# Optimization experiments

Hardware: AMD Instinct MI355X
Metric: run time of the kernel (lower is better)

## Reference

```python
import jax, jax.numpy as jnp
import numpy as np

E = 400000   # total edges
G = 64       # num graphs
H = 256      # hidden_dim
NN = 20000   # node id range
FRONTIER_BONUS = 0.5


def layer_norm(x, g, b, eps=1e-5):
    m = jnp.mean(x, axis=-1, keepdims=True)
    v = jnp.var(x, axis=-1, keepdims=True)
    return (x - m) / jnp.sqrt(v + eps) * g + b


def setup_inputs() -> dict:
    key = jax.random.key(0)
    ks = jax.random.split(key, 20)
    s = 0.02
    inp = {
        "edge_tokens": jax.random.normal(ks[0], (E, H), jnp.float32),
        "question_tokens": jax.random.normal(ks[1], (G, H), jnp.float32),
        "edge_batch": jnp.sort(jax.random.randint(ks[2], (E,), 0, G)),
        "selected_mask": jax.random.bernoulli(ks[3], 0.3, (E,)),
        "edge_heads": jax.random.randint(ks[4], (E,), 0, NN),
        "edge_tails": jax.random.randint(ks[5], (E,), 0, NN),
        "current_tail": jax.random.randint(ks[6], (G,), 0, NN),
        # edge_proj params: LayerNorm(H+2) -> Linear(H+2,H) -> GELU -> Linear(H,H) -> GELU
        "ln1_g": jnp.ones((H + 2,), jnp.float32),
        "ln1_b": jnp.zeros((H + 2,), jnp.float32),
        "W1": s * jax.random.normal(ks[7], (H + 2, H), jnp.float32),
        "b1": jnp.zeros((H,), jnp.float32),
        "W2": s * jax.random.normal(ks[8], (H, H), jnp.float32),
        "b2": jnp.zeros((H,), jnp.float32),
        # selection_head: Linear(H,1)
        "sel_w": s * jax.random.normal(ks[9], (H, 1), jnp.float32),
        "sel_b": jnp.zeros((1,), jnp.float32),
        # stop_head: LayerNorm(2H) -> Linear(2H,H) -> GELU -> Linear(H,1)
        "ln2_g": jnp.ones((2 * H,), jnp.float32),
        "ln2_b": jnp.zeros((2 * H,), jnp.float32),
        "sW1": s * jax.random.normal(ks[10], (2 * H, H), jnp.float32),
        "sb1": jnp.zeros((H,), jnp.float32),
        "sW2": s * jax.random.normal(ks[11], (H, 1), jnp.float32),
        "sb2": jnp.zeros((1,), jnp.float32),
    }
    return inp


def reference(edge_tokens, question_tokens, edge_batch, selected_mask,
              edge_heads, edge_tails, current_tail,
              ln1_g, ln1_b, W1, b1, W2, b2, sel_w, sel_b,
              ln2_g, ln2_b, sW1, sb1, sW2, sb2):
    num_graphs = question_tokens.shape[0]
    candidate = ~selected_mask
    cur_e = current_tail[edge_batch]                       # [E] gather by graph id
    frontier = candidate & ((edge_heads == cur_e) | (edge_tails == cur_e))
    aux = jnp.stack([candidate.astype(jnp.float32), frontier.astype(jnp.float32)], axis=-1)
    x = jnp.concatenate([edge_tokens, aux], axis=-1)       # [E, H+2]
    h = layer_norm(x, ln1_g, ln1_b)
    h = jax.nn.gelu(h @ W1 + b1, approximate=False)        # Dropout is identity in eval
    h = jax.nn.gelu(h @ W2 + b2, approximate=False)        # edge_repr [E, H]
    edge_logits = (h @ sel_w)[:, 0] + sel_b[0]
    edge_logits = edge_logits + FRONTIER_BONUS * frontier.astype(jnp.float32)
    counts = jax.ops.segment_sum(jnp.ones((h.shape[0],), jnp.float32), edge_batch, num_segments=num_graphs)
    counts = jnp.clip(counts, 1.0)                          # bincount.clamp(min=1)
    pooled = jax.ops.segment_sum(h, edge_batch, num_segments=num_graphs) / counts[:, None]
    s_in = jnp.concatenate([pooled, question_tokens], axis=-1)  # [G, 2H]
    s = layer_norm(s_in, ln2_g, ln2_b)
    s = jax.nn.gelu(s @ sW1 + sb1, approximate=False)
    stop_logits = (s @ sW2)[:, 0] + sb2[0]
    return edge_logits, stop_logits, pooled
```

## Files before the change

### kernel.cpp

```cpp
#include <hip/hip_runtime.h>
#include <hip/hip_bf16.h>
#include <cstdint>


typedef __bf16 bf16x8 __attribute__((ext_vector_type(8)));
typedef float  f32x4  __attribute__((ext_vector_type(4)));

__device__ __forceinline__ float gelu_f(float x) {
  float x2 = x * x;
  float t1 = __builtin_fmaf(0.1029444f, x2, 2.3022078f);
  float a  = x * t1;
  float e;
  asm("v_exp_f32 %0, %1" : "=v"(e) : "v"(a));
  float r;
  asm("v_rcp_f32 %0, %1" : "=v"(r) : "v"(e + 1.0f));
  return x - x * r;
}

__device__ __forceinline__ bf16x8 as_frag(uint4 u) {
  union { uint4 u; bf16x8 f; } c; c.u = u; return c.f;
}

__global__ void prep_pack(const float* __restrict__ W1, const float* __restrict__ W2,
                          const float* __restrict__ ln1g,
                          __bf16* __restrict__ W1p, __bf16* __restrict__ W2p) {
  int gid = blockIdx.x * blockDim.x + threadIdx.x;
  int m  = gid >> 13;
  int b  = (gid >> 6) & 127;
  int l  = gid & 63;
  int kt = b >> 4, nt = b & 15;
  int k0 = kt * 32 + ((l >> 4) << 3);
  int n  = nt * 16 + (l & 15);
  const float* W = m ? W2 : W1;
  bf16x8 v;
#pragma unroll
  for (int i = 0; i < 8; ++i) {
    int k = k0 + i;
    float wv = W[k * 256 + n];
    if (!m) wv *= ln1g[k];
    v[i] = (__bf16)wv;
  }
  __bf16* dst = m ? W2p : W1p;
  *(bf16x8*)(dst + (size_t)(b * 64 + l) * 8) = v;
}

__global__ void prep_vec(const float* __restrict__ W1, const float* __restrict__ ln1g,
                         const float* __restrict__ ln1b, const float* __restrict__ b1,
                         const unsigned* __restrict__ smask_words,
                         float* __restrict__ C0, float* __restrict__ GW6,
                         float* __restrict__ GW7, int* __restrict__ maskIsByte) {
  __shared__ float red[4][256];
  const int n = threadIdx.x & 255, c = threadIdx.x >> 8;
  const int k0 = c * 64, k1 = (c == 3) ? 258 : k0 + 64;
  float s = 0.f;
#pragma unroll 4
  for (int k = k0; k < k1; ++k) s += ln1b[k] * W1[k * 256 + n];
  red[c][n] = s;
  __syncthreads();
  if (c == 0) {
    C0[n]  = b1[n] + red[0][n] + red[1][n] + red[2][n] + red[3][n];
    GW6[n] = ln1g[256] * W1[256 * 256 + n];
    GW7[n] = ln1g[257] * W1[257 * 256 + n];
  }
  if (threadIdx.x == 0) {
    int big = 0;
    for (int i = 0; i < 64; ++i) { if (smask_words[i] > 1u) big = 1; }
    *maskIsByte = big;
  }
}

#define EPB 64

__device__ __forceinline__ void gemm8_reg(const char* __restrict__ Wp,
                                          const char* aBase, unsigned swA,
                                          unsigned gA, int bOff,
                                          f32x4 (&acc)[4][4]) {
  uint4 bv[4], bn[4];
#pragma unroll
  for (int cf = 0; cf < 4; ++cf)
    bv[cf] = *(const uint4*)(Wp + bOff + (cf << 10));
#pragma unroll
  for (int kt = 0; kt < 8; ++kt) {
    if (kt < 7) {
#pragma unroll
      for (int cf = 0; cf < 4; ++cf)
        bn[cf] = *(const uint4*)(Wp + (kt + 1) * 16384 + bOff + (cf << 10));
    }
    bf16x8 av[4];
#pragma unroll
    for (int rf = 0; rf < 4; ++rf)
      av[rf] = *(const bf16x8*)(aBase + rf * 8192 + (((unsigned)(kt * 64) + gA) ^ swA));
#pragma unroll
    for (int rf = 0; rf < 4; ++rf)
#pragma unroll
      for (int cf = 0; cf < 4; ++cf)
        acc[rf][cf] = __builtin_amdgcn_mfma_f32_16x16x32_bf16(av[rf], as_frag(bv[cf]),
                                                              acc[rf][cf], 0, 0, 0);
#pragma unroll
    for (int cf = 0; cf < 4; ++cf) bv[cf] = bn[cf];
  }
}

__global__ __launch_bounds__(256, 3) void edge_kernel(
    const float* __restrict__ tok, const int* __restrict__ ebatch,
    const unsigned char* __restrict__ smaskB,
    const int* __restrict__ eheads, const int* __restrict__ etails,
    const int* __restrict__ curtail,
    const __bf16* __restrict__ W1p, const __bf16* __restrict__ W2p,
    const float* __restrict__ C0v, const float* __restrict__ GW6v,
    const float* __restrict__ GW7v, const float* __restrict__ b2v,
    const float* __restrict__ selwv, const float* __restrict__ selbv,
    const int* __restrict__ maskFlag,
    float* __restrict__ outLogits, float* __restrict__ pooledAcc,
    float* __restrict__ cnts) {
  __shared__ __align__(16) char As_[64 * 512];
  __shared__ float sZa0[64], sZa1[64], sFront[64];
  __shared__ float sLog[64][4];
  __shared__ int sG[64];

  const int t = threadIdx.x;
  const int w = t >> 6, l = t & 63;
  const int base = blockIdx.x * EPB;

  if (t < 64) {
    int ge = base + t;
    int g  = ebatch[ge];
    int mb = *maskFlag;
    int mv = mb ? (int)smaskB[ge] : ((const int*)smaskB)[ge];
    int cand = (mv == 0);
    int cur  = curtail[g];
    int fr   = cand && ((eheads[ge] == cur) || (etails[ge] == cur));
    sZa0[t] = (float)cand; sZa1[t] = (float)fr; sFront[t] = (float)fr; sG[t] = g;
  }
  __syncthreads();

  if (t == 0) {
    int cg = sG[0]; float run = 1.f;
    for (int e = 1; e < EPB; ++e) {
      int g = sG[e];
      if (g == cg) run += 1.f;
      else { atomicAdd(&cnts[cg], run); cg = g; run = 1.f; }
    }
    atomicAdd(&cnts[cg], run);
  }

  {
    const int e = t >> 2, q = t & 3;
    const float* rp = tok + (size_t)(base + e) * 256 + q * 4;
    float s = 0.f, s2 = 0.f;
#pragma unroll
    for (int j = 0; j < 16; ++j) {
      float4 v = *(const float4*)(rp + j * 16);
      s  += v.x + v.y + v.z + v.w;
      s2 += v.x * v.x + v.y * v.y + v.z * v.z + v.w * v.w;
    }
    float a0 = 0.f, a1 = 0.f;
    if (q == 0) { a0 = sZa0[e]; a1 = sZa1[e]; s += a0 + a1; s2 += a0 + a1; }
    s  += __shfl_xor(s, 1);  s  += __shfl_xor(s, 2);
    s2 += __shfl_xor(s2, 1); s2 += __shfl_xor(s2, 2);
    const float mean = s * (1.0f / 258.0f);
    const float var  = s2 * (1.0f / 258.0f) - mean * mean;
    const float rstd = rsqrtf(var + 1e-5f);
    const float nm   = -mean * rstd;
    const unsigned sw = (unsigned)(e & 7) << 4;
    const float* rp2 = rp;
    asm volatile("" : "+v"(rp2));
#pragma unroll
    for (int j = 0; j < 16; ++j) {
      float4 v = *(const float4*)(rp2 + j * 16);
      union { __bf16 h[4]; uint2 u; } cv;
      cv.h[0] = (__bf16)__builtin_fmaf(v.x, rstd, nm);
      cv.h[1] = (__bf16)__builtin_fmaf(v.y, rstd, nm);
      cv.h[2] = (__bf16)__builtin_fmaf(v.z, rstd, nm);
      cv.h[3] = (__bf16)__builtin_fmaf(v.w, rstd, nm);
      unsigned off = (unsigned)(q * 8 + j * 32);
      *(uint2*)(As_ + e * 512 + (off ^ sw)) = cv.u;
    }
    if (q == 0) {
      sZa0[e] = __builtin_fmaf(a0, rstd, nm);
      sZa1[e] = __builtin_fmaf(a1, rstd, nm);
    }
  }
  __syncthreads();

  const int rA = l & 15;
  const int r0 = (l >> 4) << 2;
  f32x4 acc[4][4];
  {
    float c0r[4], w6r[4], w7r[4];
#pragma unroll
    for (int cf = 0; cf < 4; ++cf) {
      int col = w * 64 + cf * 16 + rA;
      c0r[cf] = C0v[col]; w6r[cf] = GW6v[col]; w7r[cf] = GW7v[col];
    }
    f32x4 za0q[4], za1q[4];
#pragma unroll
    for (int rf = 0; rf < 4; ++rf) {
      za0q[rf] = *(const f32x4*)&sZa0[rf * 16 + r0];
      za1q[rf] = *(const f32x4*)&sZa1[rf * 16 + r0];
    }
#pragma unroll
    for (int rf = 0; rf < 4; ++rf)
#pragma unroll
      for (int cf = 0; cf < 4; ++cf)
#pragma unroll
        for (int i = 0; i < 4; ++i)
          acc[rf][cf][i] = c0r[cf] + za0q[rf][i] * w6r[cf] + za1q[rf][i] * w7r[cf];
  }

  const unsigned swA = (unsigned)(rA & 7) << 4;
  const unsigned gA  = (unsigned)((l >> 4) << 4);
  const char* aBase  = As_ + rA * 512;
  const int bOff     = (w << 12) + (l << 4);

  gemm8_reg((const char*)W1p, aBase, swA, gA, bOff, acc);
  __syncthreads();

#pragma unroll
  for (int rf = 0; rf < 4; ++rf)
#pragma unroll
    for (int i = 0; i < 4; ++i) {
      int row = rf * 16 + r0 + i;
      char* rowp = As_ + row * 512;
      unsigned sw = (unsigned)(row & 7) << 4;
#pragma unroll
      for (int cf = 0; cf < 4; ++cf) {
        int col = w * 64 + cf * 16 + rA;
        *(__bf16*)(rowp + (((unsigned)(col * 2)) ^ sw)) = (__bf16)gelu_f(acc[rf][cf][i]);
      }
    }
  __syncthreads();

#pragma unroll
  for (int cf = 0; cf < 4; ++cf) {
    float bb = b2v[w * 64 + cf * 16 + rA];
#pragma unroll
    for (int rf = 0; rf < 4; ++rf)
#pragma unroll
      for (int i = 0; i < 4; ++i) acc[rf][cf][i] = bb;
  }
  gemm8_reg((const char*)W2p, aBase, swA, gA, bOff, acc);

#pragma unroll
  for (int rf = 0; rf < 4; ++rf)
#pragma unroll
    for (int cf = 0; cf < 4; ++cf)
#pragma unroll
      for (int i = 0; i < 4; ++i) acc[rf][cf][i] = gelu_f(acc[rf][cf][i]);

  {
    float lwr[4];
#pragma unroll
    for (int cf = 0; cf < 4; ++cf) lwr[cf] = selwv[w * 64 + cf * 16 + rA];
#pragma unroll
    for (int rf = 0; rf < 4; ++rf)
#pragma unroll
      for (int i = 0; i < 4; ++i) {
        float p = acc[rf][0][i] * lwr[0] + acc[rf][1][i] * lwr[1]
                + acc[rf][2][i] * lwr[2] + acc[rf][3][i] * lwr[3];
        p += __shfl_xor(p, 1); p += __shfl_xor(p, 2);
        p += __shfl_xor(p, 4); p += __shfl_xor(p, 8);
        if (rA == 0) sLog[rf * 16 + r0 + i][w] = p;
      }
  }
  __syncthreads();
  if (t < 64)
    outLogits[base + t] = sLog[t][0] + sLog[t][1] + sLog[t][2] + sLog[t][3]
                        + selbv[0] + 0.5f * sFront[t];

  if (sG[0] == sG[EPB - 1]) {
    int g = sG[0];
#pragma unroll
    for (int cf = 0; cf < 4; ++cf) {
      float sv = 0.f;
#pragma unroll
      for (int rf = 0; rf < 4; ++rf)
#pragma unroll
        for (int i = 0; i < 4; ++i) sv += acc[rf][cf][i];
      sv += __shfl_xor(sv, 16);
      sv += __shfl_xor(sv, 32);
      if (l < 16) atomicAdd(&pooledAcc[g * 256 + w * 64 + cf * 16 + l], sv);
    }
  } else {
#pragma unroll
    for (int rf = 0; rf < 4; ++rf)
#pragma unroll
      for (int i = 0; i < 4; ++i) {
        int row = rf * 16 + r0 + i;
        int g = sG[row];
#pragma unroll
        for (int cf = 0; cf < 4; ++cf)
          atomicAdd(&pooledAcc[g * 256 + w * 64 + cf * 16 + rA], acc[rf][cf][i]);
      }
  }
}

__global__ __launch_bounds__(256) void stop_kernel(
    const float* __restrict__ pooledAcc, const float* __restrict__ cnts,
    const float* __restrict__ qtok,
    const float* __restrict__ ln2g, const float* __restrict__ ln2b,
    const float* __restrict__ sW1, const float* __restrict__ sb1,
    const float* __restrict__ sW2, const float* __restrict__ sb2,
    float* __restrict__ outStop, float* __restrict__ outPooled) {
  __shared__ float sIn[512], sLn[512], sRed[8];
  const int t = threadIdx.x, g = blockIdx.x;
  const int w = t >> 6, l = t & 63;
  float c = fmaxf(cnts[g], 1.0f);
  float p = pooledAcc[g * 256 + t] / c;
  outPooled[g * 256 + t] = p;
  sIn[t] = p;
  sIn[256 + t] = qtok[g * 256 + t];
  __syncthreads();
  float a = sIn[t], b = sIn[256 + t];
  float s = a + b, s2 = a * a + b * b;
#pragma unroll
  for (int m = 1; m < 64; m <<= 1) { s += __shfl_xor(s, m); s2 += __shfl_xor(s2, m); }
  if (l == 0) { sRed[w] = s; sRed[4 + w] = s2; }
  __syncthreads();
  s  = sRed[0] + sRed[1] + sRed[2] + sRed[3];
  s2 = sRed[4] + sRed[5] + sRed[6] + sRed[7];
  const float mean = s * (1.0f / 512.0f);
  const float var  = s2 * (1.0f / 512.0f) - mean * mean;
  const float rstd = rsqrtf(var + 1e-5f);
  sLn[t]       = (a - mean) * rstd * ln2g[t] + ln2b[t];
  sLn[256 + t] = (b - mean) * rstd * ln2g[256 + t] + ln2b[256 + t];
  __syncthreads();
  float accv = sb1[t];
#pragma unroll 8
  for (int k = 0; k < 512; ++k) accv += sLn[k] * sW1[k * 256 + t];
  float u = gelu_f(accv);
  float part = u * sW2[t];
#pragma unroll
  for (int m = 1; m < 64; m <<= 1) part += __shfl_xor(part, m);
  if (l == 0) sRed[w] = part;
  __syncthreads();
  if (t == 0) outStop[g] = sRed[0] + sRed[1] + sRed[2] + sRed[3] + sb2[0];
}

extern "C" void kernel_launch(void* const* d_in, const int* in_sizes, int n_in,
                              void* d_out, int out_size, void* d_ws, size_t ws_size,
                              hipStream_t stream) {
  const float* tok   = (const float*)d_in[0];
  const float* qtok  = (const float*)d_in[1];
  const int* ebatch  = (const int*)d_in[2];
  const void* smask  = d_in[3];
  const int* eheads  = (const int*)d_in[4];
  const int* etails  = (const int*)d_in[5];
  const int* curtail = (const int*)d_in[6];
  const float* ln1g  = (const float*)d_in[7];
  const float* ln1b  = (const float*)d_in[8];
  const float* W1    = (const float*)d_in[9];
  const float* b1    = (const float*)d_in[10];
  const float* W2    = (const float*)d_in[11];
  const float* b2    = (const float*)d_in[12];
  const float* selw  = (const float*)d_in[13];
  const float* selb  = (const float*)d_in[14];
  const float* ln2g  = (const float*)d_in[15];
  const float* ln2b  = (const float*)d_in[16];
  const float* sW1   = (const float*)d_in[17];
  const float* sb1   = (const float*)d_in[18];
  const float* sW2   = (const float*)d_in[19];
  const float* sb2   = (const float*)d_in[20];

  const int E = in_sizes[2];
  const int G = in_sizes[1] / 256;

  char* ws = (char*)d_ws;
  __bf16* W1p   = (__bf16*)(ws);
  __bf16* W2p   = (__bf16*)(ws + 131072);
  float*  C0    = (float*)(ws + 262144);
  float*  GW6   = (float*)(ws + 263168);
  float*  GW7   = (float*)(ws + 264192);
  float*  pooled= (float*)(ws + 265216);
  float*  cnts  = (float*)(ws + 330752);
  int*    mflag = (int*)(ws + 331008);
  (void)ws_size; (void)n_in; (void)out_size;

  hipMemsetAsync(ws + 265216, 0, 65536 + 256, stream);

  prep_pack<<<64, 256, 0, stream>>>(W1, W2, ln1g, W1p, W2p);
  prep_vec<<<1, 1024, 0, stream>>>(W1, ln1g, ln1b, b1, (const unsigned*)smask,
                                   C0, GW6, GW7, mflag);
  edge_kernel<<<E / EPB, 256, 0, stream>>>(
      tok, ebatch, (const unsigned char*)smask, eheads, etails, curtail,
      W1p, W2p, C0, GW6, GW7, b2, selw, selb, mflag,
      (float*)d_out, pooled, cnts);
  stop_kernel<<<G, 256, 0, stream>>>(pooled, cnts, qtok, ln2g, ln2b,
                                     sW1, sb1, sW2, sb2,
                                     (float*)d_out + E, (float*)d_out + E + G);
}
```

Measured before the change: 300.5 us.

## Make edge kernel persistent and deepen weight prefetch to two k-steps

The edge kernel becomes a grid-stride persistent kernel with 768 blocks, each looping over 64-edge tiles instead of launching one block per tile. The GEMM inner loop now holds three rotating register buffers, so weight fragments are fetched two k-steps ahead rather than one. The aim is to cut block launch and teardown overhead and hide more global-load latency for the weights. The costs are more VGPRs, which could hurt occupancy at launch bounds of 3 blocks per CU, an extra barrier per tile, and no overlap between tiles within a block.

Result: slower. 764.8 us (+154.5%).

```diff
diff --git a/kernel.cpp b/kernel.cpp
--- a/kernel.cpp
+++ b/kernel.cpp
@@ -75,16 +75,25 @@
                                           const char* aBase, unsigned swA,
                                           unsigned gA, int bOff,
                                           f32x4 (&acc)[4][4]) {
-  uint4 bv[4], bn[4];
-#pragma unroll
-  for (int cf = 0; cf < 4; ++cf)
-    bv[cf] = *(const uint4*)(Wp + bOff + (cf << 10));
+  uint4 b0[4], b1_[4], b2_[4];
+#pragma unroll
+  for (int cf = 0; cf < 4; ++cf) b0[cf]  = *(const uint4*)(Wp + bOff + (cf << 10));
+#pragma unroll
+  for (int cf = 0; cf < 4; ++cf) b1_[cf] = *(const uint4*)(Wp + 16384 + bOff + (cf << 10));
 #pragma unroll
   for (int kt = 0; kt < 8; ++kt) {
-    if (kt < 7) {
-#pragma unroll
-      for (int cf = 0; cf < 4; ++cf)
-        bn[cf] = *(const uint4*)(Wp + (kt + 1) * 16384 + bOff + (cf << 10));
+    if (kt < 6) {
+      const char* pf = Wp + (size_t)(kt + 2) * 16384 + bOff;
+      if ((kt + 2) % 3 == 0) {
+#pragma unroll
+        for (int cf = 0; cf < 4; ++cf) b0[cf]  = *(const uint4*)(pf + (cf << 10));
+      } else if ((kt + 2) % 3 == 1) {
+#pragma unroll
+        for (int cf = 0; cf < 4; ++cf) b1_[cf] = *(const uint4*)(pf + (cf << 10));
+      } else {
+#pragma unroll
+        for (int cf = 0; cf < 4; ++cf) b2_[cf] = *(const uint4*)(pf + (cf << 10));
+      }
     }
     bf16x8 av[4];
 #pragma unroll
@@ -93,11 +102,11 @@
 #pragma unroll
     for (int rf = 0; rf < 4; ++rf)
 #pragma unroll
-      for (int cf = 0; cf < 4; ++cf)
-        acc[rf][cf] = __builtin_amdgcn_mfma_f32_16x16x32_bf16(av[rf], as_frag(bv[cf]),
+      for (int cf = 0; cf < 4; ++cf) {
+        bf16x8 bf = as_frag((kt % 3 == 0) ? b0[cf] : (kt % 3 == 1) ? b1_[cf] : b2_[cf]);
+        acc[rf][cf] = __builtin_amdgcn_mfma_f32_16x16x32_bf16(av[rf], bf,
                                                               acc[rf][cf], 0, 0, 0);
-#pragma unroll
-    for (int cf = 0; cf < 4; ++cf) bv[cf] = bn[cf];
+      }
   }
 }
 
@@ -112,7 +121,7 @@
     const float* __restrict__ selwv, const float* __restrict__ selbv,
     const int* __restrict__ maskFlag,
     float* __restrict__ outLogits, float* __restrict__ pooledAcc,
-    float* __restrict__ cnts) {
+    float* __restrict__ cnts, int nTiles) {
   __shared__ __align__(16) char As_[64 * 512];
   __shared__ float sZa0[64], sZa1[64], sFront[64];
   __shared__ float sLog[64][4];
@@ -120,178 +129,182 @@
 
   const int t = threadIdx.x;
   const int w = t >> 6, l = t & 63;
-  const int base = blockIdx.x * EPB;
-
-  if (t < 64) {
-    int ge = base + t;
-    int g  = ebatch[ge];
-    int mb = *maskFlag;
-    int mv = mb ? (int)smaskB[ge] : ((const int*)smaskB)[ge];
-    int cand = (mv == 0);
-    int cur  = curtail[g];
-    int fr   = cand && ((eheads[ge] == cur) || (etails[ge] == cur));
-    sZa0[t] = (float)cand; sZa1[t] = (float)fr; sFront[t] = (float)fr; sG[t] = g;
-  }
-  __syncthreads();
-
-  if (t == 0) {
-    int cg = sG[0]; float run = 1.f;
-    for (int e = 1; e < EPB; ++e) {
-      int g = sG[e];
-      if (g == cg) run += 1.f;
-      else { atomicAdd(&cnts[cg], run); cg = g; run = 1.f; }
-    }
-    atomicAdd(&cnts[cg], run);
-  }
-
-  {
-    const int e = t >> 2, q = t & 3;
-    const float* rp = tok + (size_t)(base + e) * 256 + q * 4;
-    float s = 0.f, s2 = 0.f;
-#pragma unroll
-    for (int j = 0; j < 16; ++j) {
-      float4 v = *(const float4*)(rp + j * 16);
-      s  += v.x + v.y + v.z + v.w;
-      s2 += v.x * v.x + v.y * v.y + v.z * v.z + v.w * v.w;
-    }
-    float a0 = 0.f, a1 = 0.f;
-    if (q == 0) { a0 = sZa0[e]; a1 = sZa1[e]; s += a0 + a1; s2 += a0 + a1; }
-    s  += __shfl_xor(s, 1);  s  += __shfl_xor(s, 2);
-    s2 += __shfl_xor(s2, 1); s2 += __shfl_xor(s2, 2);
-    const float mean = s * (1.0f / 258.0f);
-    const float var  = s2 * (1.0f / 258.0f) - mean * mean;
-    const float rstd = rsqrtf(var + 1e-5f);
-    const float nm   = -mean * rstd;
-    const unsigned sw = (unsigned)(e & 7) << 4;
-    const float* rp2 = rp;
-    asm volatile("" : "+v"(rp2));
-#pragma unroll
-    for (int j = 0; j < 16; ++j) {
-      float4 v = *(const float4*)(rp2 + j * 16);
-      union { __bf16 h[4]; uint2 u; } cv;
-      cv.h[0] = (__bf16)__builtin_fmaf(v.x, rstd, nm);
-      cv.h[1] = (__bf16)__builtin_fmaf(v.y, rstd, nm);
-      cv.h[2] = (__bf16)__builtin_fmaf(v.z, rstd, nm);
-      cv.h[3] = (__bf16)__builtin_fmaf(v.w, rstd, nm);
-      unsigned off = (unsigned)(q * 8 + j * 32);
-      *(uint2*)(As_ + e * 512 + (off ^ sw)) = cv.u;
-    }
-    if (q == 0) {
-      sZa0[e] = __builtin_fmaf(a0, rstd, nm);
-      sZa1[e] = __builtin_fmaf(a1, rstd, nm);
-    }
-  }
-  __syncthreads();
-
-  const int rA = l & 15;
-  const int r0 = (l >> 4) << 2;
-  f32x4 acc[4][4];
-  {
-    float c0r[4], w6r[4], w7r[4];
-#pragma unroll
-    for (int cf = 0; cf < 4; ++cf) {
-      int col = w * 64 + cf * 16 + rA;
-      c0r[cf] = C0v[col]; w6r[cf] = GW6v[col]; w7r[cf] = GW7v[col];
-    }
-    f32x4 za0q[4], za1q[4];
-#pragma unroll
-    for (int rf = 0; rf < 4; ++rf) {
-      za0q[rf] = *(const f32x4*)&sZa0[rf * 16 + r0];
-      za1q[rf] = *(const f32x4*)&sZa1[rf * 16 + r0];
-    }
-#pragma unroll
-    for (int rf = 0; rf < 4; ++rf)
-#pragma unroll
-      for (int cf = 0; cf < 4; ++cf)
-#pragma unroll
-        for (int i = 0; i < 4; ++i)
-          acc[rf][cf][i] = c0r[cf] + za0q[rf][i] * w6r[cf] + za1q[rf][i] * w7r[cf];
-  }
-
-  const unsigned swA = (unsigned)(rA & 7) << 4;
-  const unsigned gA  = (unsigned)((l >> 4) << 4);
-  const char* aBase  = As_ + rA * 512;
-  const int bOff     = (w << 12) + (l << 4);
-
-  gemm8_reg((const char*)W1p, aBase, swA, gA, bOff, acc);
-  __syncthreads();
-
-#pragma unroll
-  for (int rf = 0; rf < 4; ++rf)
-#pragma unroll
-    for (int i = 0; i < 4; ++i) {
-      int row = rf * 16 + r0 + i;
-      char* rowp = As_ + row * 512;
-      unsigned sw = (unsigned)(row & 7) << 4;
+  const int mb = *maskFlag;
+
+  for (int tile = blockIdx.x; tile < nTiles; tile += gridDim.x) {
+    const int base = tile * EPB;
+
+    if (t < 64) {
+      int ge = base + t;
+      int g  = ebatch[ge];
+      int mv = mb ? (int)smaskB[ge] : ((const int*)smaskB)[ge];
+      int cand = (mv == 0);
+      int cur  = curtail[g];
+      int fr   = cand && ((eheads[ge] == cur) || (etails[ge] == cur));
+      sZa0[t] = (float)cand; sZa1[t] = (float)fr; sFront[t] = (float)fr; sG[t] = g;
+    }
+    __syncthreads();
+
+    if (t == 0) {
+      int cg = sG[0]; float run = 1.f;
+      for (int e = 1; e < EPB; ++e) {
+        int g = sG[e];
+        if (g == cg) run += 1.f;
+        else { atomicAdd(&cnts[cg], run); cg = g; run = 1.f; }
+      }
+      atomicAdd(&cnts[cg], run);
+    }
+
+    {
+      const int e = t >> 2, q = t & 3;
+      const float* rp = tok + (size_t)(base + e) * 256 + q * 4;
+      float s = 0.f, s2 = 0.f;
+#pragma unroll
+      for (int j = 0; j < 16; ++j) {
+        float4 v = *(const float4*)(rp + j * 16);
+        s  += v.x + v.y + v.z + v.w;
+        s2 += v.x * v.x + v.y * v.y + v.z * v.z + v.w * v.w;
+      }
+      float a0 = 0.f, a1 = 0.f;
+      if (q == 0) { a0 = sZa0[e]; a1 = sZa1[e]; s += a0 + a1; s2 += a0 + a1; }
+      s  += __shfl_xor(s, 1);  s  += __shfl_xor(s, 2);
+      s2 += __shfl_xor(s2, 1); s2 += __shfl_xor(s2, 2);
+      const float mean = s * (1.0f / 258.0f);
+      const float var  = s2 * (1.0f / 258.0f) - mean * mean;
+      const float rstd = rsqrtf(var + 1e-5f);
+      const float nm   = -mean * rstd;
+      const unsigned sw = (unsigned)(e & 7) << 4;
+      const float* rp2 = rp;
+      asm volatile("" : "+v"(rp2));
+#pragma unroll
+      for (int j = 0; j < 16; ++j) {
+        float4 v = *(const float4*)(rp2 + j * 16);
+        union { __bf16 h[4]; uint2 u; } cv;
+        cv.h[0] = (__bf16)__builtin_fmaf(v.x, rstd, nm);
+        cv.h[1] = (__bf16)__builtin_fmaf(v.y, rstd, nm);
+        cv.h[2] = (__bf16)__builtin_fmaf(v.z, rstd, nm);
+        cv.h[3] = (__bf16)__builtin_fmaf(v.w, rstd, nm);
+        unsigned off = (unsigned)(q * 8 + j * 32);
+        *(uint2*)(As_ + e * 512 + (off ^ sw)) = cv.u;
+      }
+      if (q == 0) {
+        sZa0[e] = __builtin_fmaf(a0, rstd, nm);
+        sZa1[e] = __builtin_fmaf(a1, rstd, nm);
+      }
+    }
+    __syncthreads();
+
+    const int rA = l & 15;
+    const int r0 = (l >> 4) << 2;
+    f32x4 acc[4][4];
+    {
+      float c0r[4], w6r[4], w7r[4];
 #pragma unroll
       for (int cf = 0; cf < 4; ++cf) {
         int col = w * 64 + cf * 16 + rA;
-        *(__bf16*)(rowp + (((unsigned)(col * 2)) ^ sw)) = (__bf16)gelu_f(acc[rf][cf][i]);
-      }
-    }
-  __syncthreads();
-
-#pragma unroll
-  for (int cf = 0; cf < 4; ++cf) {
-    float bb = b2v[w * 64 + cf * 16 + rA];
-#pragma unroll
-    for (int rf = 0; rf < 4; ++rf)
-#pragma unroll
-      for (int i = 0; i < 4; ++i) acc[rf][cf][i] = bb;
-  }
-  gemm8_reg((const char*)W2p, aBase, swA, gA, bOff, acc);
-
-#pragma unroll
-  for (int rf = 0; rf < 4; ++rf)
-#pragma unroll
-    for (int cf = 0; cf < 4; ++cf)
-#pragma unroll
-      for (int i = 0; i < 4; ++i) acc[rf][cf][i] = gelu_f(acc[rf][cf][i]);
-
-  {
-    float lwr[4];
-#pragma unroll
-    for (int cf = 0; cf < 4; ++cf) lwr[cf] = selwv[w * 64 + cf * 16 + rA];
-#pragma unroll
-    for (int rf = 0; rf < 4; ++rf)
-#pragma unroll
-      for (int i = 0; i < 4; ++i) {
-        float p = acc[rf][0][i] * lwr[0] + acc[rf][1][i] * lwr[1]
-                + acc[rf][2][i] * lwr[2] + acc[rf][3][i] * lwr[3];
-        p += __shfl_xor(p, 1); p += __shfl_xor(p, 2);
-        p += __shfl_xor(p, 4); p += __shfl_xor(p, 8);
-        if (rA == 0) sLog[rf * 16 + r0 + i][w] = p;
-      }
-  }
-  __syncthreads();
-  if (t < 64)
-    outLogits[base + t] = sLog[t][0] + sLog[t][1] + sLog[t][2] + sLog[t][3]
-                        + selbv[0] + 0.5f * sFront[t];
-
-  if (sG[0] == sG[EPB - 1]) {
-    int g = sG[0];
-#pragma unroll
-    for (int cf = 0; cf < 4; ++cf) {
-      float sv = 0.f;
+        c0r[cf] = C0v[col]; w6r[cf] = GW6v[col]; w7r[cf] = GW7v[col];
+      }
+      f32x4 za0q[4], za1q[4];
+#pragma unroll
+      for (int rf = 0; rf < 4; ++rf) {
+        za0q[rf] = *(const f32x4*)&sZa0[rf * 16 + r0];
+        za1q[rf] = *(const f32x4*)&sZa1[rf * 16 + r0];
+      }
 #pragma unroll
       for (int rf = 0; rf < 4; ++rf)
 #pragma unroll
-        for (int i = 0; i < 4; ++i) sv += acc[rf][cf][i];
-      sv += __shfl_xor(sv, 16);
-      sv += __shfl_xor(sv, 32);
-      if (l < 16) atomicAdd(&pooledAcc[g * 256 + w * 64 + cf * 16 + l], sv);
-    }
-  } else {
+        for (int cf = 0; cf < 4; ++cf)
+#pragma unroll
+          for (int i = 0; i < 4; ++i)
+            acc[rf][cf][i] = c0r[cf] + za0q[rf][i] * w6r[cf] + za1q[rf][i] * w7r[cf];
+    }
+
+    const unsigned swA = (unsigned)(rA & 7) << 4;
+    const unsigned gA  = (unsigned)((l >> 4) << 4);
+    const char* aBase  = As_ + rA * 512;
+    const int bOff     = (w << 12) + (l << 4);
+
+    gemm8_reg((const char*)W1p, aBase, swA, gA, bOff, acc);
+    __syncthreads();
+
 #pragma unroll
     for (int rf = 0; rf < 4; ++rf)
 #pragma unroll
       for (int i = 0; i < 4; ++i) {
         int row = rf * 16 + r0 + i;
-        int g = sG[row];
-#pragma unroll
-        for (int cf = 0; cf < 4; ++cf)
-          atomicAdd(&pooledAcc[g * 256 + w * 64 + cf * 16 + rA], acc[rf][cf][i]);
-      }
+        char* rowp = As_ + row * 512;
+        unsigned sw = (unsigned)(row & 7) << 4;
+#pragma unroll
+        for (int cf = 0; cf < 4; ++cf) {
+          int col = w * 64 + cf * 16 + rA;
+          *(__bf16*)(rowp + (((unsigned)(col * 2)) ^ sw)) = (__bf16)gelu_f(acc[rf][cf][i]);
+        }
+      }
+    __syncthreads();
+
+#pragma unroll
+    for (int cf = 0; cf < 4; ++cf) {
+      float bb = b2v[w * 64 + cf * 16 + rA];
+#pragma unroll
+      for (int rf = 0; rf < 4; ++rf)
+#pragma unroll
+        for (int i = 0; i < 4; ++i) acc[rf][cf][i] = bb;
+    }
+    gemm8_reg((const char*)W2p, aBase, swA, gA, bOff, acc);
+
+#pragma unroll
+    for (int rf = 0; rf < 4; ++rf)
+#pragma unroll
+      for (int cf = 0; cf < 4; ++cf)
+#pragma unroll
+        for (int i = 0; i < 4; ++i) acc[rf][cf][i] = gelu_f(acc[rf][cf][i]);
+
+    {
+      float lwr[4];
+#pragma unroll
+      for (int cf = 0; cf < 4; ++cf) lwr[cf] = selwv[w * 64 + cf * 16 + rA];
+#pragma unroll
+      for (int rf = 0; rf < 4; ++rf)
+#pragma unroll
+        for (int i = 0; i < 4; ++i) {
+          float p = acc[rf][0][i] * lwr[0] + acc[rf][1][i] * lwr[1]
+                  + acc[rf][2][i] * lwr[2] + acc[rf][3][i] * lwr[3];
+          p += __shfl_xor(p, 1); p += __shfl_xor(p, 2);
+          p += __shfl_xor(p, 4); p += __shfl_xor(p, 8);
+          if (rA == 0) sLog[rf * 16 + r0 + i][w] = p;
+        }
+    }
+    __syncthreads();
+    if (t < 64)
+      outLogits[base + t] = sLog[t][0] + sLog[t][1] + sLog[t][2] + sLog[t][3]
+                          + selbv[0] + 0.5f * sFront[t];
+
+    if (sG[0] == sG[EPB - 1]) {
+      int g = sG[0];
+#pragma unroll
+      for (int cf = 0; cf < 4; ++cf) {
+        float sv = 0.f;
+#pragma unroll
+        for (int rf = 0; rf < 4; ++rf)
+#pragma unroll
+          for (int i = 0; i < 4; ++i) sv += acc[rf][cf][i];
+        sv += __shfl_xor(sv, 16);
+        sv += __shfl_xor(sv, 32);
+        if (l < 16) atomicAdd(&pooledAcc[g * 256 + w * 64 + cf * 16 + l], sv);
+      }
+    } else {
+#pragma unroll
+      for (int rf = 0; rf < 4; ++rf)
+#pragma unroll
+        for (int i = 0; i < 4; ++i) {
+          int row = rf * 16 + r0 + i;
+          int g = sG[row];
+#pragma unroll
+          for (int cf = 0; cf < 4; ++cf)
+            atomicAdd(&pooledAcc[g * 256 + w * 64 + cf * 16 + rA], acc[rf][cf][i]);
+        }
+    }
+    __syncthreads();
   }
 }
 
@@ -381,10 +394,10 @@
   prep_pack<<<64, 256, 0, stream>>>(W1, W2, ln1g, W1p, W2p);
   prep_vec<<<1, 1024, 0, stream>>>(W1, ln1g, ln1b, b1, (const unsigned*)smask,
                                    C0, GW6, GW7, mflag);
-  edge_kernel<<<E / EPB, 256, 0, stream>>>(
+  edge_kernel<<<768, 256, 0, stream>>>(
       tok, ebatch, (const unsigned char*)smask, eheads, etails, curtail,
       W1p, W2p, C0, GW6, GW7, b2, selw, selb, mflag,
-      (float*)d_out, pooled, cnts);
+      (float*)d_out, pooled, cnts, E / EPB);
   stop_kernel<<<G, 256, 0, stream>>>(pooled, cnts, qtok, ln2g, ln2b,
                                      sW1, sb1, sW2, sb2,
                                      (float*)d_out + E, (float*)d_out + E + G);
```

## Fold metadata prologue into LayerNorm pass and prefetch first weight tiles early

Applied to the files above, without the earlier changes.

Removes the separate 64-thread metadata phase and its barrier. The q==0 lane of each edge now computes the candidate and frontier flags and hands them to the other lanes with shuffles. The first k-tile of W1 is loaded before the LayerNorm phase, and the first W2 tile is issued before the GELU writeback, so global latency overlaps other work. The per-block count atomics move after the barrier. This costs extra registers held across the LayerNorm phase, which may reduce occupancy.

Result: slower. 311.5 us (+3.7%).

```diff
diff --git a/kernel.cpp b/kernel.cpp
--- a/kernel.cpp
+++ b/kernel.cpp
@@ -71,16 +71,13 @@
 
 #define EPB 64
 
-__device__ __forceinline__ void gemm8_reg(const char* __restrict__ Wp,
+__device__ __forceinline__ void gemm8_pre(const char* __restrict__ Wp,
                                           const char* aBase, unsigned swA,
                                           unsigned gA, int bOff,
-                                          f32x4 (&acc)[4][4]) {
-  uint4 bv[4], bn[4];
-#pragma unroll
-  for (int cf = 0; cf < 4; ++cf)
-    bv[cf] = *(const uint4*)(Wp + bOff + (cf << 10));
+                                          uint4 (&bv)[4], f32x4 (&acc)[4][4]) {
 #pragma unroll
   for (int kt = 0; kt < 8; ++kt) {
+    uint4 bn[4];
     if (kt < 7) {
 #pragma unroll
       for (int cf = 0; cf < 4; ++cf)
@@ -121,32 +118,18 @@
   const int t = threadIdx.x;
   const int w = t >> 6, l = t & 63;
   const int base = blockIdx.x * EPB;
-
-  if (t < 64) {
-    int ge = base + t;
-    int g  = ebatch[ge];
-    int mb = *maskFlag;
-    int mv = mb ? (int)smaskB[ge] : ((const int*)smaskB)[ge];
-    int cand = (mv == 0);
-    int cur  = curtail[g];
-    int fr   = cand && ((eheads[ge] == cur) || (etails[ge] == cur));
-    sZa0[t] = (float)cand; sZa1[t] = (float)fr; sFront[t] = (float)fr; sG[t] = g;
-  }
-  __syncthreads();
-
-  if (t == 0) {
-    int cg = sG[0]; float run = 1.f;
-    for (int e = 1; e < EPB; ++e) {
-      int g = sG[e];
-      if (g == cg) run += 1.f;
-      else { atomicAdd(&cnts[cg], run); cg = g; run = 1.f; }
-    }
-    atomicAdd(&cnts[cg], run);
-  }
-
+  const int bOff = (w << 12) + (l << 4);
+  const int mb = *maskFlag;
+
+  uint4 wb0[4];
+#pragma unroll
+  for (int cf = 0; cf < 4; ++cf)
+    wb0[cf] = *(const uint4*)((const char*)W1p + bOff + (cf << 10));
+
+  const int e = t >> 2, q = t & 3;
+  const int ge = base + e;
   {
-    const int e = t >> 2, q = t & 3;
-    const float* rp = tok + (size_t)(base + e) * 256 + q * 4;
+    const float* rp = tok + (size_t)ge * 256 + q * 4;
     float s = 0.f, s2 = 0.f;
 #pragma unroll
     for (int j = 0; j < 16; ++j) {
@@ -154,10 +137,21 @@
       s  += v.x + v.y + v.z + v.w;
       s2 += v.x * v.x + v.y * v.y + v.z * v.z + v.w * v.w;
     }
-    float a0 = 0.f, a1 = 0.f;
-    if (q == 0) { a0 = sZa0[e]; a1 = sZa1[e]; s += a0 + a1; s2 += a0 + a1; }
+    float candf = 0.f, frontf = 0.f;
+    if (q == 0) {
+      int g  = ebatch[ge];
+      int mv = mb ? (int)smaskB[ge] : ((const int*)smaskB)[ge];
+      int cand = (mv == 0);
+      int cur  = curtail[g];
+      int fr   = cand && ((eheads[ge] == cur) || (etails[ge] == cur));
+      candf = (float)cand; frontf = (float)fr;
+      sFront[e] = (float)fr; sG[e] = g;
+    }
+    const float a0 = __shfl(candf,  l & 60);
+    const float a1 = __shfl(frontf, l & 60);
     s  += __shfl_xor(s, 1);  s  += __shfl_xor(s, 2);
     s2 += __shfl_xor(s2, 1); s2 += __shfl_xor(s2, 2);
+    s += a0 + a1; s2 += a0 + a1;
     const float mean = s * (1.0f / 258.0f);
     const float var  = s2 * (1.0f / 258.0f) - mean * mean;
     const float rstd = rsqrtf(var + 1e-5f);
@@ -183,6 +177,16 @@
   }
   __syncthreads();
 
+  if (t == 0) {
+    int cg = sG[0]; float run = 1.f;
+    for (int ee = 1; ee < EPB; ++ee) {
+      int g = sG[ee];
+      if (g == cg) run += 1.f;
+      else { atomicAdd(&cnts[cg], run); cg = g; run = 1.f; }
+    }
+    atomicAdd(&cnts[cg], run);
+  }
+
   const int rA = l & 15;
   const int r0 = (l >> 4) << 2;
   f32x4 acc[4][4];
@@ -211,10 +215,13 @@
   const unsigned swA = (unsigned)(rA & 7) << 4;
   const unsigned gA  = (unsigned)((l >> 4) << 4);
   const char* aBase  = As_ + rA * 512;
-  const int bOff     = (w << 12) + (l << 4);
-
-  gemm8_reg((const char*)W1p, aBase, swA, gA, bOff, acc);
-  __syncthreads();
+
+  gemm8_pre((const char*)W1p, aBase, swA, gA, bOff, wb0, acc);
+  __syncthreads();
+
+#pragma unroll
+  for (int cf = 0; cf < 4; ++cf)
+    wb0[cf] = *(const uint4*)((const char*)W2p + bOff + (cf << 10));
 
 #pragma unroll
   for (int rf = 0; rf < 4; ++rf)
@@ -239,7 +246,7 @@
 #pragma unroll
       for (int i = 0; i < 4; ++i) acc[rf][cf][i] = bb;
   }
-  gemm8_reg((const char*)W2p, aBase, swA, gA, bOff, acc);
+  gemm8_pre((const char*)W2p, aBase, swA, gA, bOff, wb0, acc);
 
 #pragma unroll
   for (int rf = 0; rf < 4; ++rf)
```
